# Kernel tuning notes

Hardware: AMD Instinct MI355X
Metric: run time of the kernel (lower is better)

The kernel has to match this reference:

```python
import jax, jax.numpy as jnp
import numpy as np

N = 50000      # nodes
E = 1_600_000  # edges (avg degree 32)
IN, H, OUT, R = 128, 64, 32, 8
NEG_SLOPE = 0.2


def _rgat(x, src, dst, etype, W, q, k, b, n_nodes):
    """PyG RGATConv, defaults: heads=1, dim=1, additive-self-attention,
    across-relation softmax, concat=True, bias=True, dropout=0 (eval)."""
    # per-relation transform of all nodes: [R, N, O] (cheaper than per-edge bmm since 2*deg >> R)
    t = jnp.einsum('ni,rio->rno', x, W)
    xi = t[etype, dst]                      # [E, O] transformed target feats
    xj = t[etype, src]                      # [E, O] transformed source feats
    a = (xi @ q + xj @ k)[:, 0]             # [E] additive attention logits
    a = jnp.where(a >= 0, a, NEG_SLOPE * a)  # leaky_relu
    # segment softmax over incoming edges of each target node (across relations)
    m = jax.ops.segment_max(a, dst, num_segments=n_nodes)
    m = jnp.where(jnp.isfinite(m), m, 0.0)
    ex = jnp.exp(a - m[dst])
    s = jax.ops.segment_sum(ex, dst, num_segments=n_nodes)
    alpha = ex / (s[dst] + 1e-16)
    out = jax.ops.segment_sum(alpha[:, None] * xj, dst, num_segments=n_nodes)
    return out + b


def setup_inputs() -> dict:
    key = jax.random.key(0)
    ks = jax.random.split(key, 24)
    x = jax.random.normal(ks[0], (N, IN), jnp.float32)
    edge_index = jax.random.randint(ks[1], (2, E), 0, N, jnp.int32)
    edge_type = jax.random.randint(ks[2], (E,), 0, R, jnp.int32)

    def glorot(k, shape, fan_in):
        return jax.random.normal(k, shape, jnp.float32) * (1.0 / np.sqrt(fan_in))

    d = dict(x=x, edge_index=edge_index, edge_type=edge_type)
    # conv1: in->hidden, conv_mu / conv_logvar: hidden->hidden
    d['W1'] = glorot(ks[3], (R, IN, H), IN)
    d['q1'] = glorot(ks[4], (H, 1), H)
    d['k1'] = glorot(ks[5], (H, 1), H)
    d['b1'] = jnp.zeros((H,), jnp.float32)
    d['Wmu'] = glorot(ks[6], (R, H, H), H)
    d['qmu'] = glorot(ks[7], (H, 1), H)
    d['kmu'] = glorot(ks[8], (H, 1), H)
    d['bmu'] = jnp.zeros((H,), jnp.float32)
    d['Wlv'] = glorot(ks[9], (R, H, H), H)
    d['qlv'] = glorot(ks[10], (H, 1), H)
    d['klv'] = glorot(ks[11], (H, 1), H)
    d['blv'] = jnp.zeros((H,), jnp.float32)
    d['Wm'] = glorot(ks[12], (H, OUT), H)   # linear_mu (stored [in,out])
    d['bm'] = jnp.zeros((OUT,), jnp.float32)
    d['Wl'] = glorot(ks[13], (H, OUT), H)   # linear_logvar
    d['bl'] = jnp.zeros((OUT,), jnp.float32)
    return d


def reference(x, edge_index, edge_type, W1, q1, k1, b1,
              Wmu, qmu, kmu, bmu, Wlv, qlv, klv, blv, Wm, bm, Wl, bl):
    src, dst = edge_index[0], edge_index[1]
    hidden = jax.nn.relu(_rgat(x, src, dst, edge_type, W1, q1, k1, b1, N))
    mu = jax.nn.relu(_rgat(hidden, src, dst, edge_type, Wmu, qmu, kmu, bmu, N))
    mu = mu @ Wm + bm                       # dropout is identity in eval
    logvar = jax.nn.relu(_rgat(hidden, src, dst, edge_type, Wlv, qlv, klv, blv, N))
    logvar = logvar @ Wl + bl
    logstd = 0.5 * logvar
    return (mu, logstd)
```

## Files before the change

### kernel.cpp

```cpp
#include <hip/hip_runtime.h>
#include <cstdint>

#define HDIM 64
#define ODIM 32
#define NEG_SLOPE 0.2f
#define SCHUNK 2048

__device__ __forceinline__ unsigned f2bf_rne(float f) {
  unsigned u = __float_as_uint(f);
  return (u + 0x7FFFu + ((u >> 16) & 1u)) >> 16;
}

__device__ __forceinline__ unsigned fenc(float f) {
  unsigned u = __float_as_uint(f);
  return (u & 0x80000000u) ? ~u : (u | 0x80000000u);
}
__device__ __forceinline__ float fdec(unsigned e) {
  unsigned u = (e & 0x80000000u) ? (e ^ 0x80000000u) : ~e;
  return __uint_as_float(u);
}

__global__ __launch_bounds__(256) void count_deg_kernel(
    const int* __restrict__ dst, int* __restrict__ deg, int E) {
  int e = blockIdx.x * 256 + threadIdx.x;
  if (e < E) atomicAdd(&deg[dst[e]], 1);
}

__global__ __launch_bounds__(256) void scan_p1(const int* __restrict__ deg,
                                               int* __restrict__ bsum, int n) {
  int base = blockIdx.x * SCHUNK + threadIdx.x * 8;
  int s = 0;
#pragma unroll
  for (int j = 0; j < 8; j++) {
    int i = base + j;
    if (i < n) s += deg[i];
  }
#pragma unroll
  for (int d = 1; d < 64; d <<= 1) s += __shfl_xor(s, d, 64);
  __shared__ int ws[4];
  if ((threadIdx.x & 63) == 0) ws[threadIdx.x >> 6] = s;
  __syncthreads();
  if (threadIdx.x == 0) bsum[blockIdx.x] = ws[0] + ws[1] + ws[2] + ws[3];
}

__global__ void scan_p2(int* bsum, int nb) {
  int i = threadIdx.x;
  int v = (i < nb) ? bsum[i] : 0;
  int orig = v;
#pragma unroll
  for (int d = 1; d < 64; d <<= 1) {
    int up = __shfl_up(v, d, 64);
    if (i >= d) v += up;
  }
  if (i < nb) bsum[i] = v - orig;
}

__global__ __launch_bounds__(256) void scan_p3(const int* __restrict__ deg,
                                               const int* __restrict__ bsum,
                                               int* __restrict__ row_ptr,
                                               int n) {
  int base = blockIdx.x * SCHUNK + threadIdx.x * 8;
  int vals[8];
  int s = 0;
#pragma unroll
  for (int j = 0; j < 8; j++) {
    int i = base + j;
    vals[j] = (i < n) ? deg[i] : 0;
    s += vals[j];
  }
  int lane = threadIdx.x & 63, w = threadIdx.x >> 6;
  int v = s;
#pragma unroll
  for (int d = 1; d < 64; d <<= 1) {
    int up = __shfl_up(v, d, 64);
    if (lane >= d) v += up;
  }
  __shared__ int wsum[4];
  if (lane == 63) wsum[w] = v;
  __syncthreads();
  int woff = 0;
#pragma unroll
  for (int i = 0; i < 4; i++) woff += (i < w) ? wsum[i] : 0;
  int off = bsum[blockIdx.x] + woff + v - s;
#pragma unroll
  for (int j = 0; j < 8; j++) {
    int i = base + j;
    off += vals[j];
    if (i < n) row_ptr[i + 1] = off;
  }
  if (blockIdx.x == 0 && threadIdx.x == 0) row_ptr[0] = 0;
}

__global__ __launch_bounds__(256) void scatter_kernel(
    const int* __restrict__ src, const int* __restrict__ dst,
    const int* __restrict__ etype, const int* __restrict__ row_ptr,
    int* __restrict__ fill, int* __restrict__ edges, int E) {
  int e = blockIdx.x * 256 + threadIdx.x;
  if (e < E) {
    int d = dst[e];
    int pos = row_ptr[d] + atomicAdd(&fill[d], 1);
    edges[pos] = src[e] | (etype[e] << 16);
  }
}

__global__ __launch_bounds__(256) void rowmax_kernel(
    const float* __restrict__ ak, unsigned* __restrict__ maxk_enc, int N) {
  const int row = blockIdx.x;
  const int nchunks = gridDim.y;
  const int per = (N + nchunks - 1) / nchunks;
  const int beg = blockIdx.y * per;
  const int end = min(N, beg + per);
  const float* r = ak + (size_t)row * N;
  float m = -1e30f;
  for (int i = beg + threadIdx.x; i < end; i += 256) m = fmaxf(m, r[i]);
#pragma unroll
  for (int d = 1; d < 64; d <<= 1) m = fmaxf(m, __shfl_xor(m, d, 64));
  __shared__ float ws[4];
  if ((threadIdx.x & 63) == 0) ws[threadIdx.x >> 6] = m;
  __syncthreads();
  if (threadIdx.x == 0) {
    float bm = fmaxf(fmaxf(ws[0], ws[1]), fmaxf(ws[2], ws[3]));
    atomicMax(&maxk_enc[row], fenc(bm));
  }
}

template <int CIN>
__global__ __launch_bounds__(256) void transform_kernel(
    const float* __restrict__ f, const float* __restrict__ W,
    const float* __restrict__ q, const float* __restrict__ k,
    unsigned short* __restrict__ tb, float* __restrict__ aq,
    float* __restrict__ ak, int N) {
  constexpr int KC = 16;
  constexpr int FLD = 260;
  constexpr int WLD = 68;
  __shared__ float Fl[KC * FLD];
  __shared__ float Wl[KC * WLD];

  const int r = blockIdx.x;
  const int n0 = blockIdx.y * 256;
  const int tid = threadIdx.x;
  const int nt = tid >> 3;
  const int ot = tid & 7;
  const int on0 = ot * 8;

  float acc[8][8];
#pragma unroll
  for (int i = 0; i < 8; i++)
#pragma unroll
    for (int j = 0; j < 8; j++) acc[i][j] = 0.f;

  for (int k0 = 0; k0 < CIN; k0 += KC) {
    {
      const int kk = (tid & 3) * 4;
      const int nb = tid >> 2;
#pragma unroll
      for (int i = 0; i < 4; i++) {
        const int n = nb + i * 64;
        const int gn = n0 + n;
        float4 v = make_float4(0.f, 0.f, 0.f, 0.f);
        if (gn < N) v = *(const float4*)&f[(size_t)gn * CIN + k0 + kk];
        Fl[(kk + 0) * FLD + n] = v.x;
        Fl[(kk + 1) * FLD + n] = v.y;
        Fl[(kk + 2) * FLD + n] = v.z;
        Fl[(kk + 3) * FLD + n] = v.w;
      }
    }
    {
      const int oc = (tid & 15) * 4;
      const int kr = tid >> 4;
      float4 v = *(const float4*)&W[((size_t)r * CIN + k0 + kr) * 64 + oc];
      *(float4*)&Wl[kr * WLD + oc] = v;
    }
    __syncthreads();

#pragma unroll 4
    for (int kk = 0; kk < KC; kk++) {
      float4 fA = *(const float4*)&Fl[kk * FLD + nt * 8];
      float4 fB = *(const float4*)&Fl[kk * FLD + nt * 8 + 4];
      float4 wA = *(const float4*)&Wl[kk * WLD + on0];
      float4 wB = *(const float4*)&Wl[kk * WLD + on0 + 4];
      float fv[8] = {fA.x, fA.y, fA.z, fA.w, fB.x, fB.y, fB.z, fB.w};
      float wv[8] = {wA.x, wA.y, wA.z, wA.w, wB.x, wB.y, wB.z, wB.w};
#pragma unroll
      for (int i = 0; i < 8; i++)
#pragma unroll
        for (int j = 0; j < 8; j++) acc[i][j] = fmaf(fv[i], wv[j], acc[i][j]);
    }
    __syncthreads();
  }

  float qv[8], kv[8];
#pragma unroll
  for (int j = 0; j < 8; j++) {
    qv[j] = q[on0 + j];
    kv[j] = k[on0 + j];
  }

#pragma unroll
  for (int i = 0; i < 8; i++) {
    const int gn = n0 + nt * 8 + i;
    const bool valid = gn < N;
    if (valid) {
      unsigned pk[4];
#pragma unroll
      for (int j = 0; j < 4; j++)
        pk[j] = f2bf_rne(acc[i][2 * j]) | (f2bf_rne(acc[i][2 * j + 1]) << 16);
      *(uint4*)&tb[((size_t)r * N + gn) * 64 + on0] =
          make_uint4(pk[0], pk[1], pk[2], pk[3]);
    }
    float vq = 0.f, vk = 0.f;
#pragma unroll
    for (int j = 0; j < 8; j++) {
      vq = fmaf(acc[i][j], qv[j], vq);
      vk = fmaf(acc[i][j], kv[j], vk);
    }
#pragma unroll
    for (int d = 1; d < 8; d <<= 1) {
      vq += __shfl_xor(vq, d, 64);
      vk += __shfl_xor(vk, d, 64);
    }
    if (ot == 0 && valid) {
      aq[(size_t)r * N + gn] = vq;
      ak[(size_t)r * N + gn] = vk;
    }
  }
}

__global__ __launch_bounds__(256) void transform2_kernel(
    const float* __restrict__ f, const float* __restrict__ Wa,
    const float* __restrict__ Wb, const float* __restrict__ qa,
    const float* __restrict__ ka, const float* __restrict__ qb,
    const float* __restrict__ kb, unsigned* __restrict__ t2p,
    float* __restrict__ aq2, float* __restrict__ ak2, int N) {
  constexpr int CIN = 64, KC = 16;
  constexpr int FLD = 132;
  constexpr int WLD = 68;
  __shared__ float Fl[KC * FLD];
  __shared__ float Wl[2][KC * WLD + 4];

  const int r = blockIdx.x;
  const int n0 = blockIdx.y * 128;
  const int tid = threadIdx.x;
  const int nt = tid >> 4;
  const int ot = tid & 15;
  const int mat = ot >> 3;
  const int on0 = (ot & 7) * 8;

  float acc[8][8];
#pragma unroll
  for (int i = 0; i < 8; i++)
#pragma unroll
    for (int j = 0; j < 8; j++) acc[i][j] = 0.f;

  for (int k0 = 0; k0 < CIN; k0 += KC) {
    {
      const int kk = (tid & 3) * 4;
      const int nb = tid >> 2;
#pragma unroll
      for (int i = 0; i < 2; i++) {
        const int n = nb + i * 64;
        const int gn = n0 + n;
        float4 v = make_float4(0.f, 0.f, 0.f, 0.f);
        if (gn < N) v = *(const float4*)&f[(size_t)gn * CIN + k0 + kk];
        Fl[(kk + 0) * FLD + n] = v.x;
        Fl[(kk + 1) * FLD + n] = v.y;
        Fl[(kk + 2) * FLD + n] = v.z;
        Fl[(kk + 3) * FLD + n] = v.w;
      }
    }
    {
      const int oc = (tid & 15) * 4;
      const int kr = tid >> 4;
      float4 va = *(const float4*)&Wa[((size_t)r * CIN + k0 + kr) * 64 + oc];
      float4 vb = *(const float4*)&Wb[((size_t)r * CIN + k0 + kr) * 64 + oc];
      *(float4*)&Wl[0][kr * WLD + oc] = va;
      *(float4*)&Wl[1][kr * WLD + oc] = vb;
    }
    __syncthreads();

#pragma unroll 4
    for (int kk = 0; kk < KC; kk++) {
      float4 fA = *(const float4*)&Fl[kk * FLD + nt * 8];
      float4 fB = *(const float4*)&Fl[kk * FLD + nt * 8 + 4];
      float4 wA = *(const float4*)&Wl[mat][kk * WLD + on0];
      float4 wB = *(const float4*)&Wl[mat][kk * WLD + on0 + 4];
      float fv[8] = {fA.x, fA.y, fA.z, fA.w, fB.x, fB.y, fB.z, fB.w};
      float wv[8] = {wA.x, wA.y, wA.z, wA.w, wB.x, wB.y, wB.z, wB.w};
#pragma unroll
      for (int i = 0; i < 8; i++)
#pragma unroll
        for (int j = 0; j < 8; j++) acc[i][j] = fmaf(fv[i], wv[j], acc[i][j]);
    }
    __syncthreads();
  }

  const float* qsel = mat ? qb : qa;
  const float* ksel = mat ? kb : ka;
  float qv[8], kv[8];
#pragma unroll
  for (int j = 0; j < 8; j++) {
    qv[j] = qsel[on0 + j];
    kv[j] = ksel[on0 + j];
  }

#pragma unroll
  for (int i = 0; i < 8; i++) {
    const int gn = n0 + nt * 8 + i;
    const bool valid = gn < N;

    unsigned pk[8];
#pragma unroll
    for (int j = 0; j < 8; j++) {
      const float other = __shfl_xor(acc[i][j], 8, 64);
      pk[j] = f2bf_rne(acc[i][j]) | (f2bf_rne(other) << 16);
    }
    if (mat == 0 && valid) {
      unsigned* dst = t2p + ((size_t)r * N + gn) * 64 + on0;
      *(uint4*)dst = make_uint4(pk[0], pk[1], pk[2], pk[3]);
      *(uint4*)(dst + 4) = make_uint4(pk[4], pk[5], pk[6], pk[7]);
    }

    float vq = 0.f, vk = 0.f;
#pragma unroll
    for (int j = 0; j < 8; j++) {
      vq = fmaf(acc[i][j], qv[j], vq);
      vk = fmaf(acc[i][j], kv[j], vk);
    }
#pragma unroll
    for (int d = 1; d < 8; d <<= 1) {
      vq += __shfl_xor(vq, d, 64);
      vk += __shfl_xor(vk, d, 64);
    }
    if ((ot & 7) == 0 && valid) {
      aq2[(size_t)(mat * 8 + r) * N + gn] = vq;
      ak2[(size_t)(mat * 8 + r) * N + gn] = vk;
    }
  }
}

__global__ __launch_bounds__(256) void aggregate_kernel(
    const int* __restrict__ row_ptr, const int* __restrict__ edges,
    const unsigned short* __restrict__ tb, const float* __restrict__ aq,
    const float* __restrict__ ak, const unsigned* __restrict__ maxk_enc,
    const float* __restrict__ bias, float* __restrict__ out, int N) {
  const int tid = threadIdx.x;
  const int w = tid >> 6, o = tid & 63;
  int wid = blockIdx.x * 4 + w;
  const bool valid = wid < N;
  if (!valid) wid = N - 1;
  const int beg = row_ptr[wid];
  const int end = valid ? row_ptr[wid + 1] : beg;
  const int deg = end - beg;

  const float aqw = aq[(size_t)(o & 7) * N + wid];

  float v = aqw + fdec(maxk_enc[o & 7]);
  v = (v >= 0.f) ? v : NEG_SLOPE * v;
#pragma unroll
  for (int d = 1; d < 8; d <<= 1) v = fmaxf(v, __shfl_xor(v, d, 64));
  const float m = __shfl(v, 0, 64);

  float s = 0.f, acc = 0.f;
  for (int base = 0; base < deg; base += 64) {
    const int j = base + o;
    const int gcount = min(64, deg - base);
    const int packed = edges[beg + min(j, deg - 1)];
    const int src = packed & 0xFFFF;
    const int rr = packed >> 16;
    const int idx = rr * N + src;
    float x = __shfl(aqw, rr, 64) + ak[idx];
    x = (x >= 0.f) ? x : NEG_SLOPE * x;
    const float p = (j < deg) ? __expf(x - m) : 0.f;
    s += p;
    const int g8 = (gcount + 7) & ~7;
    for (int u = 0; u < g8; u += 8) {
      float pu[8];
      int iu[8];
#pragma unroll
      for (int q = 0; q < 8; q++) {
        pu[q] = __shfl(p, u + q, 64);
        iu[q] = __shfl(idx, u + q, 64);
      }
      unsigned short tv[8];
#pragma unroll
      for (int q = 0; q < 8; q++) tv[q] = tb[(size_t)iu[q] * 64 + o];
#pragma unroll
      for (int q = 0; q < 8; q++)
        acc = fmaf(pu[q], __uint_as_float((unsigned)tv[q] << 16), acc);
    }
  }
#pragma unroll
  for (int d = 1; d < 64; d <<= 1) s += __shfl_xor(s, d, 64);

  if (valid) {
    const float res = acc / (s + 1e-16f) + bias[o];
    out[(size_t)wid * 64 + o] = fmaxf(res, 0.f);
  }
}

__global__ __launch_bounds__(256) void aggregate2_kernel(
    const int* __restrict__ row_ptr, const int* __restrict__ edges,
    const unsigned* __restrict__ t2p, const float* __restrict__ aq2,
    const float* __restrict__ ak2, const unsigned* __restrict__ maxk2_enc,
    const float* __restrict__ bmu, const float* __restrict__ blv,
    const float* __restrict__ Wm, const float* __restrict__ bm,
    const float* __restrict__ Wlin, const float* __restrict__ bl,
    float* __restrict__ out_mu, float* __restrict__ out_ls, int N) {
  __shared__ float WmL[2048];
  __shared__ float WlL[2048];
  __shared__ float bL[64];
  __shared__ float hL[4][130];
  const int tid = threadIdx.x;
  for (int i = tid; i < 2048; i += 256) {
    WmL[i] = Wm[i];
    WlL[i] = Wlin[i];
  }
  if (tid < 32) {
    bL[tid] = bm[tid];
    bL[32 + tid] = bl[tid];
  }
  __syncthreads();

  const int w = tid >> 6, o = tid & 63;
  int wid = blockIdx.x * 4 + w;
  const bool valid = wid < N;
  if (!valid) wid = N - 1;
  const int beg = row_ptr[wid];
  const int end = valid ? row_ptr[wid + 1] : beg;
  const int deg = end - beg;

  const float aqw = aq2[(size_t)(o & 15) * N + wid];

  float v = aqw + fdec(maxk2_enc[o & 15]);
  v = (v >= 0.f) ? v : NEG_SLOPE * v;
#pragma unroll
  for (int d = 1; d < 8; d <<= 1) v = fmaxf(v, __shfl_xor(v, d, 64));
  const float m0 = __shfl(v, 0, 64);
  const float m1 = __shfl(v, 8, 64);

  float s0 = 0.f, s1 = 0.f, acc0 = 0.f, acc1 = 0.f;
  for (int base = 0; base < deg; base += 64) {
    const int j = base + o;
    const int gcount = min(64, deg - base);
    const int packed = edges[beg + min(j, deg - 1)];
    const int src = packed & 0xFFFF;
    const int rr = packed >> 16;
    const int idx = rr * N + src;
    float x0 = __shfl(aqw, rr, 64) + ak2[idx];
    float x1 = __shfl(aqw, 8 + rr, 64) + ak2[idx + 8 * N];
    x0 = (x0 >= 0.f) ? x0 : NEG_SLOPE * x0;
    x1 = (x1 >= 0.f) ? x1 : NEG_SLOPE * x1;
    const float p0 = (j < deg) ? __expf(x0 - m0) : 0.f;
    const float p1 = (j < deg) ? __expf(x1 - m1) : 0.f;
    s0 += p0;
    s1 += p1;
    const int g8 = (gcount + 7) & ~7;
    for (int u = 0; u < g8; u += 8) {
      float pu0[8], pu1[8];
      int iu[8];
#pragma unroll
      for (int q = 0; q < 8; q++) {
        pu0[q] = __shfl(p0, u + q, 64);
        pu1[q] = __shfl(p1, u + q, 64);
        iu[q] = __shfl(idx, u + q, 64);
      }
      unsigned pk[8];
#pragma unroll
      for (int q = 0; q < 8; q++) pk[q] = t2p[(size_t)iu[q] * 64 + o];
#pragma unroll
      for (int q = 0; q < 8; q++) {
        acc0 = fmaf(pu0[q], __uint_as_float(pk[q] << 16), acc0);
        acc1 = fmaf(pu1[q], __uint_as_float(pk[q] & 0xFFFF0000u), acc1);
      }
    }
  }
#pragma unroll
  for (int d = 1; d < 64; d <<= 1) {
    s0 += __shfl_xor(s0, d, 64);
    s1 += __shfl_xor(s1, d, 64);
  }

  const float h0 = fmaxf(acc0 / (s0 + 1e-16f) + bmu[o], 0.f);
  const float h1 = fmaxf(acc1 / (s1 + 1e-16f) + blv[o], 0.f);
  hL[w][o] = h0;
  hL[w][64 + o] = h1;
  __syncthreads();

  const float* hrow = &hL[w][(o >= 32) ? 64 : 0];
  const float* WL = (o >= 32) ? WlL : WmL;
  const int j = o & 31;
  float acc = 0.f;
#pragma unroll 8
  for (int c = 0; c < 64; c++) acc = fmaf(hrow[c], WL[c * 32 + j], acc);
  if (valid) {
    if (o < 32)
      out_mu[(size_t)wid * 32 + j] = acc + bL[j];
    else
      out_ls[(size_t)wid * 32 + j] = (acc + bL[32 + j]) * 0.5f;
  }
}

extern "C" void kernel_launch(void* const* d_in, const int* in_sizes, int n_in,
                              void* d_out, int out_size, void* d_ws,
                              size_t ws_size, hipStream_t stream) {
  const float* x = (const float*)d_in[0];
  const int* edge_index = (const int*)d_in[1];
  const int* edge_type = (const int*)d_in[2];
  const float* W1 = (const float*)d_in[3];
  const float* q1 = (const float*)d_in[4];
  const float* k1 = (const float*)d_in[5];
  const float* b1 = (const float*)d_in[6];
  const float* Wmu = (const float*)d_in[7];
  const float* qmu = (const float*)d_in[8];
  const float* kmu = (const float*)d_in[9];
  const float* bmu = (const float*)d_in[10];
  const float* Wlv = (const float*)d_in[11];
  const float* qlv = (const float*)d_in[12];
  const float* klv = (const float*)d_in[13];
  const float* blv = (const float*)d_in[14];
  const float* Wm = (const float*)d_in[15];
  const float* bm = (const float*)d_in[16];
  const float* Wl = (const float*)d_in[17];
  const float* bl = (const float*)d_in[18];

  const int N = in_sizes[0] / 128;
  const int E = in_sizes[2];
  const int R = in_sizes[3] / (128 * 64);

  float* out_mu = (float*)d_out;
  float* out_ls = (float*)d_out + (size_t)N * ODIM;

  char* wsp = (char*)d_ws;
  size_t off = 0;
  auto carve = [&](size_t bytes) {
    void* p = wsp + off;
    off += (bytes + 255) & ~(size_t)255;
    return p;
  };

  void* tbuf = carve((size_t)R * N * 64 * sizeof(unsigned));
  unsigned short* t1b = (unsigned short*)tbuf;
  unsigned* t2p = (unsigned*)tbuf;
  float* aq2 = (float*)carve((size_t)2 * R * N * sizeof(float));
  float* ak2 = (float*)carve((size_t)2 * R * N * sizeof(float));
  float* hidden = (float*)carve((size_t)N * HDIM * sizeof(float));
  unsigned* maxk_enc = (unsigned*)carve(2 * R * sizeof(unsigned));
  int* deg = (int*)carve((size_t)N * sizeof(int));
  int* fill = (int*)carve((size_t)N * sizeof(int));
  int* row_ptr = (int*)carve((size_t)(N + 1) * sizeof(int));
  int* bsum = (int*)carve(256 * sizeof(int));
  int* edges = (int*)carve((size_t)E * sizeof(int));

  const int* e_src = edge_index;
  const int* e_dst = edge_index + E;

  hipMemsetAsync(deg, 0, (size_t)N * sizeof(int), stream);
  hipMemsetAsync(fill, 0, (size_t)N * sizeof(int), stream);
  hipMemsetAsync(maxk_enc, 0, 2 * R * sizeof(unsigned), stream);
  count_deg_kernel<<<(E + 255) / 256, 256, 0, stream>>>(e_dst, deg, E);
  const int nchunk = (N + SCHUNK - 1) / SCHUNK;
  scan_p1<<<nchunk, 256, 0, stream>>>(deg, bsum, N);
  scan_p2<<<1, 64, 0, stream>>>(bsum, nchunk);
  scan_p3<<<nchunk, 256, 0, stream>>>(deg, bsum, row_ptr, N);
  scatter_kernel<<<(E + 255) / 256, 256, 0, stream>>>(e_src, e_dst, edge_type,
                                                      row_ptr, fill, edges, E);

  const int tiles256 = (N + 255) / 256;
  const int agg_blocks = (N + 3) / 4;

  transform_kernel<128><<<dim3(R, tiles256), 256, 0, stream>>>(
      x, W1, q1, k1, t1b, aq2, ak2, N);
  rowmax_kernel<<<dim3(R, 32), 256, 0, stream>>>(ak2, maxk_enc, N);
  aggregate_kernel<<<agg_blocks, 256, 0, stream>>>(
      row_ptr, edges, t1b, aq2, ak2, maxk_enc, b1, hidden, N);

  hipMemsetAsync(maxk_enc, 0, 2 * R * sizeof(unsigned), stream);

  const int tiles128 = (N + 127) / 128;
  transform2_kernel<<<dim3(R, tiles128), 256, 0, stream>>>(
      hidden, Wmu, Wlv, qmu, kmu, qlv, klv, t2p, aq2, ak2, N);
  rowmax_kernel<<<dim3(2 * R, 32), 256, 0, stream>>>(ak2, maxk_enc, N);
  aggregate2_kernel<<<agg_blocks, 256, 0, stream>>>(
      row_ptr, edges, t2p, aq2, ak2, maxk_enc, bmu, blv, Wm, bm, Wl, bl,
      out_mu, out_ls, N);
}
```

Baseline: 643.0 us.

## Use bf16 MFMA for per-relation transforms with bf16 inputs and hidden

Replaces the FP32 FMA-tiled transform kernels with MFMA 16x16x32 bf16 kernels. x is converted to bf16 and the weights are transposed to bf16 in small pre-pass kernels, and the hidden activations are now written as bf16. Results are staged through LDS so the t-buffer stores stay coalesced. This trades extra precision loss in the inputs, weights and hidden for much higher matmul throughput and less memory traffic, at the cost of two additional kernel launches.

Result: faster. 617.2 us (-4.0%).

```diff
diff --git a/kernel.cpp b/kernel.cpp
--- a/kernel.cpp
+++ b/kernel.cpp
@@ -6,6 +6,9 @@
 #define NEG_SLOPE 0.2f
 #define SCHUNK 2048
 
+typedef __attribute__((ext_vector_type(8))) short v8s;
+typedef __attribute__((ext_vector_type(4))) float v4f;
+
 __device__ __forceinline__ unsigned f2bf_rne(float f) {
   unsigned u = __float_as_uint(f);
   return (u + 0x7FFFu + ((u >> 16) & 1u)) >> 16;
@@ -18,6 +21,44 @@
 __device__ __forceinline__ float fdec(unsigned e) {
   unsigned u = (e & 0x80000000u) ? (e ^ 0x80000000u) : ~e;
   return __uint_as_float(u);
+}
+
+__global__ __launch_bounds__(256) void cvt_bf16_kernel(
+    const float* __restrict__ in, unsigned short* __restrict__ out, int n) {
+  int i = (blockIdx.x * 256 + threadIdx.x) * 4;
+  if (i + 3 < n) {
+    float4 v = *(const float4*)&in[i];
+    ushort4 o;
+    o.x = (unsigned short)f2bf_rne(v.x);
+    o.y = (unsigned short)f2bf_rne(v.y);
+    o.z = (unsigned short)f2bf_rne(v.z);
+    o.w = (unsigned short)f2bf_rne(v.w);
+    *(ushort4*)&out[i] = o;
+  }
+}
+
+__global__ __launch_bounds__(256) void transpose_w_kernel(
+    const float* __restrict__ W1, const float* __restrict__ Wmu,
+    const float* __restrict__ Wlv, unsigned short* __restrict__ W1t,
+    unsigned short* __restrict__ Wmut, unsigned short* __restrict__ Wlvt) {
+  const int b = blockIdx.x;
+  const int r = b & 7;
+  const int which = b >> 3;
+  const float* src;
+  unsigned short* dst;
+  int K;
+  if (which == 0) {
+    src = W1; dst = W1t; K = 128;
+  } else if (which == 1) {
+    src = Wmu; dst = Wmut; K = 64;
+  } else {
+    src = Wlv; dst = Wlvt; K = 64;
+  }
+  for (int idx = threadIdx.x; idx < K * 64; idx += 256) {
+    const int kk = idx >> 6, o = idx & 63;
+    dst[((size_t)r * 64 + o) * K + kk] =
+        (unsigned short)f2bf_rne(src[((size_t)r * K + kk) * 64 + o]);
+  }
 }
 
 __global__ __launch_bounds__(256) void count_deg_kernel(
@@ -124,217 +165,163 @@
   }
 }
 
-template <int CIN>
-__global__ __launch_bounds__(256) void transform_kernel(
-    const float* __restrict__ f, const float* __restrict__ W,
-    const float* __restrict__ q, const float* __restrict__ k,
-    unsigned short* __restrict__ tb, float* __restrict__ aq,
-    float* __restrict__ ak, int N) {
-  constexpr int KC = 16;
-  constexpr int FLD = 260;
-  constexpr int WLD = 68;
-  __shared__ float Fl[KC * FLD];
-  __shared__ float Wl[KC * WLD];
-
+__global__ __launch_bounds__(256) void transform1_mfma(
+    const unsigned short* __restrict__ xb,
+    const unsigned short* __restrict__ W1t, const float* __restrict__ q,
+    const float* __restrict__ k, unsigned short* __restrict__ tb,
+    float* __restrict__ aq, float* __restrict__ ak, int N) {
+  __shared__ unsigned short st[4][16][72];
   const int r = blockIdx.x;
-  const int n0 = blockIdx.y * 256;
   const int tid = threadIdx.x;
-  const int nt = tid >> 3;
-  const int ot = tid & 7;
-  const int on0 = ot * 8;
-
-  float acc[8][8];
-#pragma unroll
-  for (int i = 0; i < 8; i++)
-#pragma unroll
-    for (int j = 0; j < 8; j++) acc[i][j] = 0.f;
-
-  for (int k0 = 0; k0 < CIN; k0 += KC) {
-    {
-      const int kk = (tid & 3) * 4;
-      const int nb = tid >> 2;
-#pragma unroll
-      for (int i = 0; i < 4; i++) {
-        const int n = nb + i * 64;
-        const int gn = n0 + n;
-        float4 v = make_float4(0.f, 0.f, 0.f, 0.f);
-        if (gn < N) v = *(const float4*)&f[(size_t)gn * CIN + k0 + kk];
-        Fl[(kk + 0) * FLD + n] = v.x;
-        Fl[(kk + 1) * FLD + n] = v.y;
-        Fl[(kk + 2) * FLD + n] = v.z;
-        Fl[(kk + 3) * FLD + n] = v.w;
-      }
-    }
-    {
-      const int oc = (tid & 15) * 4;
-      const int kr = tid >> 4;
-      float4 v = *(const float4*)&W[((size_t)r * CIN + k0 + kr) * 64 + oc];
-      *(float4*)&Wl[kr * WLD + oc] = v;
-    }
-    __syncthreads();
-
-#pragma unroll 4
-    for (int kk = 0; kk < KC; kk++) {
-      float4 fA = *(const float4*)&Fl[kk * FLD + nt * 8];
-      float4 fB = *(const float4*)&Fl[kk * FLD + nt * 8 + 4];
-      float4 wA = *(const float4*)&Wl[kk * WLD + on0];
-      float4 wB = *(const float4*)&Wl[kk * WLD + on0 + 4];
-      float fv[8] = {fA.x, fA.y, fA.z, fA.w, fB.x, fB.y, fB.z, fB.w};
-      float wv[8] = {wA.x, wA.y, wA.z, wA.w, wB.x, wB.y, wB.z, wB.w};
-#pragma unroll
-      for (int i = 0; i < 8; i++)
-#pragma unroll
-        for (int j = 0; j < 8; j++) acc[i][j] = fmaf(fv[i], wv[j], acc[i][j]);
-    }
-    __syncthreads();
-  }
-
-  float qv[8], kv[8];
-#pragma unroll
-  for (int j = 0; j < 8; j++) {
-    qv[j] = q[on0 + j];
-    kv[j] = k[on0 + j];
-  }
-
-#pragma unroll
-  for (int i = 0; i < 8; i++) {
-    const int gn = n0 + nt * 8 + i;
-    const bool valid = gn < N;
-    if (valid) {
-      unsigned pk[4];
-#pragma unroll
-      for (int j = 0; j < 4; j++)
-        pk[j] = f2bf_rne(acc[i][2 * j]) | (f2bf_rne(acc[i][2 * j + 1]) << 16);
-      *(uint4*)&tb[((size_t)r * N + gn) * 64 + on0] =
-          make_uint4(pk[0], pk[1], pk[2], pk[3]);
-    }
+  const int w = tid >> 6;
+  const int lane = tid & 63;
+  const int quad = lane >> 4;
+  const int mrow = lane & 15;
+  const int n0w = blockIdx.y * 64 + w * 16;
+
+  const int gA = min(n0w + mrow, N - 1);
+  const unsigned short* arow = xb + (size_t)gA * 128 + quad * 8;
+  const unsigned short* wrow = W1t + ((size_t)r * 64 + mrow) * 128 + quad * 8;
+
+  v4f acc[4];
+#pragma unroll
+  for (int tt = 0; tt < 4; tt++) acc[tt] = (v4f){0.f, 0.f, 0.f, 0.f};
+
+#pragma unroll
+  for (int k0 = 0; k0 < 128; k0 += 32) {
+    v8s a = *(const v8s*)(arow + k0);
+#pragma unroll
+    for (int tt = 0; tt < 4; tt++) {
+      v8s b = *(const v8s*)(wrow + (size_t)tt * 16 * 128 + k0);
+      acc[tt] = __builtin_amdgcn_mfma_f32_16x16x32_bf16(a, b, acc[tt], 0, 0, 0);
+    }
+  }
+
+  float qv[4], kv[4];
+#pragma unroll
+  for (int tt = 0; tt < 4; tt++) {
+    qv[tt] = q[tt * 16 + mrow];
+    kv[tt] = k[tt * 16 + mrow];
+  }
+
+#pragma unroll
+  for (int i = 0; i < 4; i++) {
     float vq = 0.f, vk = 0.f;
 #pragma unroll
-    for (int j = 0; j < 8; j++) {
-      vq = fmaf(acc[i][j], qv[j], vq);
-      vk = fmaf(acc[i][j], kv[j], vk);
-    }
-#pragma unroll
-    for (int d = 1; d < 8; d <<= 1) {
+    for (int tt = 0; tt < 4; tt++) {
+      vq = fmaf(acc[tt][i], qv[tt], vq);
+      vk = fmaf(acc[tt][i], kv[tt], vk);
+      st[w][quad * 4 + i][tt * 16 + mrow] =
+          (unsigned short)f2bf_rne(acc[tt][i]);
+    }
+#pragma unroll
+    for (int d = 1; d < 16; d <<= 1) {
       vq += __shfl_xor(vq, d, 64);
       vk += __shfl_xor(vk, d, 64);
     }
-    if (ot == 0 && valid) {
+    const int gn = n0w + quad * 4 + i;
+    if (mrow == 0 && gn < N) {
       aq[(size_t)r * N + gn] = vq;
       ak[(size_t)r * N + gn] = vk;
     }
   }
-}
-
-__global__ __launch_bounds__(256) void transform2_kernel(
-    const float* __restrict__ f, const float* __restrict__ Wa,
-    const float* __restrict__ Wb, const float* __restrict__ qa,
+  __syncthreads();
+
+  const int row = lane >> 2, cg = lane & 3;
+  const int gns = n0w + row;
+  if (gns < N) {
+    const uint4 v0 = *(const uint4*)&st[w][row][cg * 16];
+    const uint4 v1 = *(const uint4*)&st[w][row][cg * 16 + 8];
+    uint4* dst = (uint4*)&tb[((size_t)r * N + gns) * 64 + cg * 16];
+    dst[0] = v0;
+    dst[1] = v1;
+  }
+}
+
+__global__ __launch_bounds__(256) void transform2_mfma(
+    const unsigned short* __restrict__ hb,
+    const unsigned short* __restrict__ Wmut,
+    const unsigned short* __restrict__ Wlvt, const float* __restrict__ qa,
     const float* __restrict__ ka, const float* __restrict__ qb,
     const float* __restrict__ kb, unsigned* __restrict__ t2p,
     float* __restrict__ aq2, float* __restrict__ ak2, int N) {
-  constexpr int CIN = 64, KC = 16;
-  constexpr int FLD = 132;
-  constexpr int WLD = 68;
-  __shared__ float Fl[KC * FLD];
-  __shared__ float Wl[2][KC * WLD + 4];
-
+  __shared__ unsigned st2[4][16][68];
   const int r = blockIdx.x;
-  const int n0 = blockIdx.y * 128;
   const int tid = threadIdx.x;
-  const int nt = tid >> 4;
-  const int ot = tid & 15;
-  const int mat = ot >> 3;
-  const int on0 = (ot & 7) * 8;
-
-  float acc[8][8];
-#pragma unroll
-  for (int i = 0; i < 8; i++)
-#pragma unroll
-    for (int j = 0; j < 8; j++) acc[i][j] = 0.f;
-
-  for (int k0 = 0; k0 < CIN; k0 += KC) {
-    {
-      const int kk = (tid & 3) * 4;
-      const int nb = tid >> 2;
-#pragma unroll
-      for (int i = 0; i < 2; i++) {
-        const int n = nb + i * 64;
-        const int gn = n0 + n;
-        float4 v = make_float4(0.f, 0.f, 0.f, 0.f);
-        if (gn < N) v = *(const float4*)&f[(size_t)gn * CIN + k0 + kk];
-        Fl[(kk + 0) * FLD + n] = v.x;
-        Fl[(kk + 1) * FLD + n] = v.y;
-        Fl[(kk + 2) * FLD + n] = v.z;
-        Fl[(kk + 3) * FLD + n] = v.w;
-      }
-    }
-    {
-      const int oc = (tid & 15) * 4;
-      const int kr = tid >> 4;
-      float4 va = *(const float4*)&Wa[((size_t)r * CIN + k0 + kr) * 64 + oc];
-      float4 vb = *(const float4*)&Wb[((size_t)r * CIN + k0 + kr) * 64 + oc];
-      *(float4*)&Wl[0][kr * WLD + oc] = va;
-      *(float4*)&Wl[1][kr * WLD + oc] = vb;
-    }
-    __syncthreads();
-
-#pragma unroll 4
-    for (int kk = 0; kk < KC; kk++) {
-      float4 fA = *(const float4*)&Fl[kk * FLD + nt * 8];
-      float4 fB = *(const float4*)&Fl[kk * FLD + nt * 8 + 4];
-      float4 wA = *(const float4*)&Wl[mat][kk * WLD + on0];
-      float4 wB = *(const float4*)&Wl[mat][kk * WLD + on0 + 4];
-      float fv[8] = {fA.x, fA.y, fA.z, fA.w, fB.x, fB.y, fB.z, fB.w};
-      float wv[8] = {wA.x, wA.y, wA.z, wA.w, wB.x, wB.y, wB.z, wB.w};
-#pragma unroll
-      for (int i = 0; i < 8; i++)
-#pragma unroll
-        for (int j = 0; j < 8; j++) acc[i][j] = fmaf(fv[i], wv[j], acc[i][j]);
-    }
-    __syncthreads();
-  }
-
-  const float* qsel = mat ? qb : qa;
-  const float* ksel = mat ? kb : ka;
-  float qv[8], kv[8];
-#pragma unroll
-  for (int j = 0; j < 8; j++) {
-    qv[j] = qsel[on0 + j];
-    kv[j] = ksel[on0 + j];
-  }
-
-#pragma unroll
-  for (int i = 0; i < 8; i++) {
-    const int gn = n0 + nt * 8 + i;
-    const bool valid = gn < N;
-
-    unsigned pk[8];
-#pragma unroll
-    for (int j = 0; j < 8; j++) {
-      const float other = __shfl_xor(acc[i][j], 8, 64);
-      pk[j] = f2bf_rne(acc[i][j]) | (f2bf_rne(other) << 16);
-    }
-    if (mat == 0 && valid) {
-      unsigned* dst = t2p + ((size_t)r * N + gn) * 64 + on0;
-      *(uint4*)dst = make_uint4(pk[0], pk[1], pk[2], pk[3]);
-      *(uint4*)(dst + 4) = make_uint4(pk[4], pk[5], pk[6], pk[7]);
-    }
-
-    float vq = 0.f, vk = 0.f;
-#pragma unroll
-    for (int j = 0; j < 8; j++) {
-      vq = fmaf(acc[i][j], qv[j], vq);
-      vk = fmaf(acc[i][j], kv[j], vk);
-    }
-#pragma unroll
-    for (int d = 1; d < 8; d <<= 1) {
-      vq += __shfl_xor(vq, d, 64);
-      vk += __shfl_xor(vk, d, 64);
-    }
-    if ((ot & 7) == 0 && valid) {
-      aq2[(size_t)(mat * 8 + r) * N + gn] = vq;
-      ak2[(size_t)(mat * 8 + r) * N + gn] = vk;
-    }
+  const int w = tid >> 6;
+  const int lane = tid & 63;
+  const int quad = lane >> 4;
+  const int mrow = lane & 15;
+  const int n0w = blockIdx.y * 64 + w * 16;
+
+  const int gA = min(n0w + mrow, N - 1);
+  const unsigned short* arow = hb + (size_t)gA * 64 + quad * 8;
+  const size_t woff = ((size_t)r * 64 + mrow) * 64 + quad * 8;
+
+  v4f am[4], al[4];
+#pragma unroll
+  for (int tt = 0; tt < 4; tt++) {
+    am[tt] = (v4f){0.f, 0.f, 0.f, 0.f};
+    al[tt] = (v4f){0.f, 0.f, 0.f, 0.f};
+  }
+
+#pragma unroll
+  for (int k0 = 0; k0 < 64; k0 += 32) {
+    v8s a = *(const v8s*)(arow + k0);
+#pragma unroll
+    for (int tt = 0; tt < 4; tt++) {
+      v8s bm = *(const v8s*)(Wmut + woff + (size_t)tt * 16 * 64 + k0);
+      v8s bl = *(const v8s*)(Wlvt + woff + (size_t)tt * 16 * 64 + k0);
+      am[tt] = __builtin_amdgcn_mfma_f32_16x16x32_bf16(a, bm, am[tt], 0, 0, 0);
+      al[tt] = __builtin_amdgcn_mfma_f32_16x16x32_bf16(a, bl, al[tt], 0, 0, 0);
+    }
+  }
+
+  float qmv[4], kmv[4], qlv2[4], klv2[4];
+#pragma unroll
+  for (int tt = 0; tt < 4; tt++) {
+    qmv[tt] = qa[tt * 16 + mrow];
+    kmv[tt] = ka[tt * 16 + mrow];
+    qlv2[tt] = qb[tt * 16 + mrow];
+    klv2[tt] = kb[tt * 16 + mrow];
+  }
+
+#pragma unroll
+  for (int i = 0; i < 4; i++) {
+    float vqm = 0.f, vkm = 0.f, vql = 0.f, vkl = 0.f;
+#pragma unroll
+    for (int tt = 0; tt < 4; tt++) {
+      vqm = fmaf(am[tt][i], qmv[tt], vqm);
+      vkm = fmaf(am[tt][i], kmv[tt], vkm);
+      vql = fmaf(al[tt][i], qlv2[tt], vql);
+      vkl = fmaf(al[tt][i], klv2[tt], vkl);
+      st2[w][quad * 4 + i][tt * 16 + mrow] =
+          f2bf_rne(am[tt][i]) | (f2bf_rne(al[tt][i]) << 16);
+    }
+#pragma unroll
+    for (int d = 1; d < 16; d <<= 1) {
+      vqm += __shfl_xor(vqm, d, 64);
+      vkm += __shfl_xor(vkm, d, 64);
+      vql += __shfl_xor(vql, d, 64);
+      vkl += __shfl_xor(vkl, d, 64);
+    }
+    const int gn = n0w + quad * 4 + i;
+    if (mrow == 0 && gn < N) {
+      aq2[(size_t)r * N + gn] = vqm;
+      ak2[(size_t)r * N + gn] = vkm;
+      aq2[(size_t)(8 + r) * N + gn] = vql;
+      ak2[(size_t)(8 + r) * N + gn] = vkl;
+    }
+  }
+  __syncthreads();
+
+  const int row = lane >> 2, cg = lane & 3;
+  const int gns = n0w + row;
+  if (gns < N) {
+    unsigned* dst = &t2p[((size_t)r * N + gns) * 64 + cg * 16];
+#pragma unroll
+    for (int s = 0; s < 4; s++)
+      *(uint4*)(dst + s * 4) = *(const uint4*)&st2[w][row][cg * 16 + s * 4];
   }
 }
 
@@ -342,7 +329,7 @@
     const int* __restrict__ row_ptr, const int* __restrict__ edges,
     const unsigned short* __restrict__ tb, const float* __restrict__ aq,
     const float* __restrict__ ak, const unsigned* __restrict__ maxk_enc,
-    const float* __restrict__ bias, float* __restrict__ out, int N) {
+    const float* __restrict__ bias, unsigned short* __restrict__ hb, int N) {
   const int tid = threadIdx.x;
   const int w = tid >> 6, o = tid & 63;
   int wid = blockIdx.x * 4 + w;
@@ -394,7 +381,7 @@
 
   if (valid) {
     const float res = acc / (s + 1e-16f) + bias[o];
-    out[(size_t)wid * 64 + o] = fmaxf(res, 0.f);
+    hb[(size_t)wid * 64 + o] = (unsigned short)f2bf_rne(fmaxf(res, 0.f));
   }
 }
 
@@ -541,9 +528,13 @@
   void* tbuf = carve((size_t)R * N * 64 * sizeof(unsigned));
   unsigned short* t1b = (unsigned short*)tbuf;
   unsigned* t2p = (unsigned*)tbuf;
+  unsigned short* xb = (unsigned short*)carve((size_t)N * 128 * 2);
+  unsigned short* hb = (unsigned short*)carve((size_t)N * 64 * 2);
+  unsigned short* W1t = (unsigned short*)carve((size_t)R * 64 * 128 * 2);
+  unsigned short* Wmut = (unsigned short*)carve((size_t)R * 64 * 64 * 2);
+  unsigned short* Wlvt = (unsigned short*)carve((size_t)R * 64 * 64 * 2);
   float* aq2 = (float*)carve((size_t)2 * R * N * sizeof(float));
   float* ak2 = (float*)carve((size_t)2 * R * N * sizeof(float));
-  float* hidden = (float*)carve((size_t)N * HDIM * sizeof(float));
   unsigned* maxk_enc = (unsigned*)carve(2 * R * sizeof(unsigned));
   int* deg = (int*)carve((size_t)N * sizeof(int));
   int* fill = (int*)carve((size_t)N * sizeof(int));
@@ -553,6 +544,10 @@
 
   const int* e_src = edge_index;
   const int* e_dst = edge_index + E;
+
+  cvt_bf16_kernel<<<(N * 128 / 4 + 255) / 256, 256, 0, stream>>>(x, xb,
+                                                                 N * 128);
+  transpose_w_kernel<<<3 * R, 256, 0, stream>>>(W1, Wmu, Wlv, W1t, Wmut, Wlvt);
 
   hipMemsetAsync(deg, 0, (size_t)N * sizeof(int), stream);
   hipMemsetAsync(fill, 0, (size_t)N * sizeof(int), stream);
@@ -565,20 +560,19 @@
   scatter_kernel<<<(E + 255) / 256, 256, 0, stream>>>(e_src, e_dst, edge_type,
                                                       row_ptr, fill, edges, E);
 
-  const int tiles256 = (N + 255) / 256;
+  const int nb64 = (N + 63) / 64;
   const int agg_blocks = (N + 3) / 4;
 
-  transform_kernel<128><<<dim3(R, tiles256), 256, 0, stream>>>(
-      x, W1, q1, k1, t1b, aq2, ak2, N);
+  transform1_mfma<<<dim3(R, nb64), 256, 0, stream>>>(xb, W1t, q1, k1, t1b,
+                                                     aq2, ak2, N);
   rowmax_kernel<<<dim3(R, 32), 256, 0, stream>>>(ak2, maxk_enc, N);
   aggregate_kernel<<<agg_blocks, 256, 0, stream>>>(
-      row_ptr, edges, t1b, aq2, ak2, maxk_enc, b1, hidden, N);
+      row_ptr, edges, t1b, aq2, ak2, maxk_enc, b1, hb, N);
 
   hipMemsetAsync(maxk_enc, 0, 2 * R * sizeof(unsigned), stream);
 
-  const int tiles128 = (N + 127) / 128;
-  transform2_kernel<<<dim3(R, tiles128), 256, 0, stream>>>(
-      hidden, Wmu, Wlv, qmu, kmu, qlv, klv, t2p, aq2, ak2, N);
+  transform2_mfma<<<dim3(R, nb64), 256, 0, stream>>>(
+      hb, Wmut, Wlvt, qmu, kmu, qlv, klv, t2p, aq2, ak2, N);
   rowmax_kernel<<<dim3(2 * R, 32), 256, 0, stream>>>(ak2, maxk_enc, N);
   aggregate2_kernel<<<agg_blocks, 256, 0, stream>>>(
       row_ptr, edges, t2p, aq2, ak2, maxk_enc, bmu, blv, Wm, bm, Wl, bl,
```
